# Kernel optimization log

Hardware: AMD Instinct MI355X
Metric: run time of the kernel (lower is better)

## Reference

```python
import jax, jax.numpy as jnp
import numpy as np

T_FINAL = 1.0
DT_STEP = 0.2
MSQ = 0.1
ALPHA = 0.0
CLIP = 1e8


def dt_to_matrix(dt):
    # dt: (H, W, 3) -> per-pixel 3x3 stencil weights (H, W, 1, 9)
    dt00 = dt
    dt01 = jnp.roll(dt00, 1, axis=1)
    dt10 = jnp.roll(dt00, 1, axis=0)
    dt11 = jnp.roll(dt01, 1, axis=0)
    dt_10 = jnp.roll(dt00, -1, axis=0)
    dt0_1 = jnp.roll(dt00, -1, axis=1)
    dt_1_1 = jnp.roll(dt_10, -1, axis=1)
    dt_11 = jnp.roll(dt_10, 1, axis=1)
    dt1_1 = jnp.roll(dt0_1, 1, axis=0)
    a00, c00, b00 = jnp.split(dt00, 3, axis=-1)
    a01, c01, b01 = jnp.split(dt01, 3, axis=-1)
    a10, c10, b10 = jnp.split(dt10, 3, axis=-1)
    a11, c11, b11 = jnp.split(dt11, 3, axis=-1)
    a0_1, c0_1, b0_1 = jnp.split(dt0_1, 3, axis=-1)
    a_10, c_10, b_10 = jnp.split(dt_10, 3, axis=-1)
    a_1_1, c_1_1, b_1_1 = jnp.split(dt_1_1, 3, axis=-1)
    a_11, c_11, b_11 = jnp.split(dt_11, 3, axis=-1)
    a1_1, c1_1, b1_1 = jnp.split(dt1_1, 3, axis=-1)
    A0 = (jnp.abs(b_11) - b_11 + jnp.abs(b00) - b00) / 4.0
    A1 = (c01 + c00 - jnp.abs(b01) - jnp.abs(b00)) / 2.0
    A2 = (jnp.abs(b11) + b11 + jnp.abs(b00) + b00) / 4.0
    A3 = (a_10 + a00 - jnp.abs(b_10) - jnp.abs(b00)) / 2.0
    A4 = (-(a_10 + 2 * a00 + a10) / 2.0
          - (jnp.abs(b_11) - b_11 + jnp.abs(b11) + b11) / 4.0
          - (jnp.abs(b_1_1) + b_1_1 + jnp.abs(b1_1) - b1_1) / 4.0
          + (jnp.abs(b_10) + jnp.abs(b10) + jnp.abs(b0_1) + jnp.abs(b01) + 2 * jnp.abs(b00)) / 2.0
          - (c0_1 + 2 * c00 + c01) / 2.0)
    A5 = (a10 + a00 - jnp.abs(b10) - jnp.abs(b00)) / 2.0
    A6 = (jnp.abs(b_1_1) + b_1_1 + jnp.abs(b00) + b00) / 4.0
    A7 = (c0_1 + c00 - jnp.abs(b0_1) - jnp.abs(b00)) / 2.0
    A8 = (jnp.abs(b1_1) - b1_1 + jnp.abs(b00) - b00) / 4.0
    return jnp.stack([A0, A1, A2, A3, A4, A5, A6, A7, A8], axis=-1)


def LB(dt, X):
    # per-pixel local 3x3 conv applied independently to each of the N channels
    A = dt_to_matrix(dt)  # (H, W, 1, 9)
    return jax.lax.conv_general_dilated_local(
        X[jnp.newaxis, ...], A, filter_shape=(3, 3), window_strides=(1, 1),
        padding='SAME', dimension_numbers=('CHWN', 'HWOI', 'CHWN'))[0]


def derivative(u):
    # forward finite differences via roll: (2, H, W, N)
    return jnp.stack([jnp.roll(u, -1, axis=0) - u, jnp.roll(u, -1, axis=1) - u])


def nrm(dt, v):
    # quadratic form: a*vx^2 + 2*b*vx*vy + c*vy^2, dt=(H,W,3), v=(2,H,W)
    return dt[:, :, 0] * v[0] ** 2 + 2 * dt[:, :, 2] * (v[1] * v[0]) + dt[:, :, 1] * v[1] ** 2


nrm2 = jax.vmap(nrm, in_axes=[None, -1], out_axes=-1)


def Pi_0(x):
    # projection onto zero-mean (simplex tangent) over channel axis
    return x - jnp.mean(x, axis=-1, keepdims=True)


def setup_inputs() -> dict:
    key = jax.random.key(0)
    k1, k2, k3, k4 = jax.random.split(key, 4)
    H, W, N = 512, 512, 48
    v = jax.random.normal(k1, (H, W, N), dtype=jnp.float32)
    Dt = jax.random.uniform(k2, (H, W, 3), dtype=jnp.float32)
    dg = jax.random.uniform(k3, (H, W, 1), dtype=jnp.float32) * 0.9 + 0.1
    hinv = jax.random.uniform(k4, (H, W, 3), dtype=jnp.float32)
    return {"v": v, "Dt": Dt, "dg": dg, "hinv": hinv}


def reference(v, Dt, dg, hinv):
    n_steps = int(T_FINAL / DT_STEP)  # 5 unrolled Euler steps

    def rhs(x):
        logp = jax.nn.log_softmax(x, axis=-1)
        val = LB(Dt, x) / dg + (1.0 - ALPHA) / 2.0 * nrm2(hinv, derivative(logp)) + MSQ * x
        return jnp.clip(Pi_0(val), -CLIP, CLIP)

    x = v
    for _ in range(n_steps):
        x = x + DT_STEP * rhs(x)
    return x
```

## Files before the change

### kernel.cpp

```cpp
#include <hip/hip_runtime.h>
#include <math.h>

#define HH 512
#define WW 512
#define NCH 48
#define HWPIX (HH * WW)

#define TW 16
#define TH 8
#define HW_HALO 18
#define HH_HALO 10
#define NHALO (HW_HALO * HH_HALO)
#define PSTRIDE 13
#define ASTRIDE 12

__global__ __launch_bounds__(256) void compute_A_kernel(
    const float* __restrict__ Dt, const float* __restrict__ dg,
    float* __restrict__ A) {
  int pix = blockIdx.x * blockDim.x + threadIdx.x;
  int h = pix >> 9;
  int w = pix & (WW - 1);
  int hm = (h == 0) ? HH - 1 : h - 1;
  int hp = (h == HH - 1) ? 0 : h + 1;
  int wm = (w == 0) ? WW - 1 : w - 1;
  int wp = (w == WW - 1) ? 0 : w + 1;

  float aC, cC, bC, cL, bL, cR, bR, aU, bU, aD, bD;
  float bUL, bUR, bDL, bDR;
  {
    int p;
    p = (h * WW + w) * 3;   aC = Dt[p]; cC = Dt[p + 1]; bC = Dt[p + 2];
    p = (h * WW + wm) * 3;  cL = Dt[p + 1]; bL = Dt[p + 2];
    p = (h * WW + wp) * 3;  cR = Dt[p + 1]; bR = Dt[p + 2];
    p = (hm * WW + w) * 3;  aU = Dt[p]; bU = Dt[p + 2];
    p = (hp * WW + w) * 3;  aD = Dt[p]; bD = Dt[p + 2];
    p = (hm * WW + wm) * 3; bUL = Dt[p + 2];
    p = (hm * WW + wp) * 3; bUR = Dt[p + 2];
    p = (hp * WW + wm) * 3; bDL = Dt[p + 2];
    p = (hp * WW + wp) * 3; bDR = Dt[p + 2];
  }

  float A0 = (fabsf(bDL) - bDL + fabsf(bC) - bC) * 0.25f;
  float A1 = (cL + cC - fabsf(bL) - fabsf(bC)) * 0.5f;
  float A2 = (fabsf(bUL) + bUL + fabsf(bC) + bC) * 0.25f;
  float A3 = (aD + aC - fabsf(bD) - fabsf(bC)) * 0.5f;
  float A4 = -(aD + 2.f * aC + aU) * 0.5f
             - (fabsf(bDL) - bDL + fabsf(bUL) + bUL) * 0.25f
             - (fabsf(bDR) + bDR + fabsf(bUR) - bUR) * 0.25f
             + (fabsf(bD) + fabsf(bU) + fabsf(bR) + fabsf(bL) + 2.f * fabsf(bC)) * 0.5f
             - (cR + 2.f * cC + cL) * 0.5f;
  float A5 = (aU + aC - fabsf(bU) - fabsf(bC)) * 0.5f;
  float A6 = (fabsf(bDR) + bDR + fabsf(bC) + bC) * 0.25f;
  float A7 = (cR + cC - fabsf(bR) - fabsf(bC)) * 0.5f;
  float A8 = (fabsf(bUR) - bUR + fabsf(bC) - bC) * 0.25f;

  bool ru = (h > 0), rd = (h < HH - 1), cl = (w > 0), cr = (w < WW - 1);
  if (!(ru && cl)) A0 = 0.f;
  if (!ru)         A1 = 0.f;
  if (!(ru && cr)) A2 = 0.f;
  if (!cl)         A3 = 0.f;
  if (!cr)         A5 = 0.f;
  if (!(rd && cl)) A6 = 0.f;
  if (!rd)         A7 = 0.f;
  if (!(rd && cr)) A8 = 0.f;

  float g = 1.0f / dg[pix];
  float4* Ao = (float4*)A + (size_t)pix * 3;
  Ao[0] = make_float4(A0 * g, A1 * g, A2 * g, A3 * g);
  Ao[1] = make_float4(A4 * g + 0.1f, A5 * g, A6 * g, A7 * g);
  Ao[2] = make_float4(A8 * g, 0.f, 0.f, 0.f);
}

__global__ __launch_bounds__(256, 4) void step_fused_kernel(
    const float* __restrict__ x, const float* __restrict__ A,
    const float* __restrict__ hinv, float* __restrict__ xn) {
  __shared__ float4 tile[NHALO * PSTRIDE];
  __shared__ float lse_s[NHALO];

  int b = blockIdx.x;
  int tile_id = (b & 7) * 256 + (b >> 3);
  int th0 = (tile_id >> 5) * TH;
  int tw0 = (tile_id & 31) * TW;

  int t = threadIdx.x;
  int sub = t & 3;
  int pair = t >> 2;
  int pr = pair >> 3;
  int pc0 = (pair & 7) * 2;
  int pix0 = (th0 + pr) * WW + (tw0 + pc0);
  int pix1 = pix0 + 1;

  float4 v[12];
  bool stager = (t < NHALO);
  if (stager) {
    int r = t / HW_HALO;
    int c = t - r * HW_HALO;
    int gh = (th0 + r - 1) & (HH - 1);
    int gw = (tw0 + c - 1) & (WW - 1);
    const float4* src = (const float4*)x + (size_t)(gh * WW + gw) * 12;
#pragma unroll
    for (int i = 0; i < 12; i++) v[i] = src[i];
  }

  const float4* ap0 = (const float4*)A + (size_t)pix0 * 3;
  const float4* ap1 = (const float4*)A + (size_t)pix1 * 3;
  float4 wA0 = ap0[0], wB0 = ap0[1], wC0 = ap0[2];
  float4 wA1 = ap1[0], wB1 = ap1[1], wC1 = ap1[2];
  const float2* hp = (const float2*)(hinv + (size_t)pix0 * 3);
  float2 h01 = hp[0], h23 = hp[1], h45 = hp[2];

  if (stager) {
    float4 mv = v[0];
#pragma unroll
    for (int i = 1; i < 12; i++) {
      mv.x = fmaxf(mv.x, v[i].x); mv.y = fmaxf(mv.y, v[i].y);
      mv.z = fmaxf(mv.z, v[i].z); mv.w = fmaxf(mv.w, v[i].w);
    }
    float m = fmaxf(fmaxf(mv.x, mv.y), fmaxf(mv.z, mv.w));
    float sx = 0.f, sy = 0.f, sz = 0.f, sw = 0.f;
#pragma unroll
    for (int i = 0; i < 12; i++) {
      sx += __expf(v[i].x - m); sy += __expf(v[i].y - m);
      sz += __expf(v[i].z - m); sw += __expf(v[i].w - m);
      tile[t * PSTRIDE + i] = v[i];
    }
    lse_s[t] = m + __logf((sx + sy) + (sz + sw));
  }
  __syncthreads();

  float wt0[9] = {wA0.x, wA0.y, wA0.z, wA0.w, wB0.x, wB0.y, wB0.z, wB0.w, wC0.x};
  float wt1[9] = {wA1.x, wA1.y, wA1.z, wA1.w, wB1.x, wB1.y, wB1.z, wB1.w, wC1.x};
  float ha0 = h01.x, hc0 = h01.y, hb0 = h23.x;
  float ha1 = h23.y, hc1 = h45.x, hb1 = h45.y;

  int lc0 = (pr + 1) * HW_HALO + (pc0 + 1);
  float l0C = lse_s[lc0];
  float l0R = lse_s[lc0 + 1];
  float l1R = lse_s[lc0 + 2];
  float l0D = lse_s[lc0 + HW_HALO];
  float l1D = lse_s[lc0 + HW_HALO + 1];
  float dld0 = l0C - l0D, dlr0 = l0C - l0R;
  float dld1 = l0R - l1D, dlr1 = l0R - l1R;

  int poff[3][4];
#pragma unroll
  for (int dr = 0; dr < 3; dr++)
#pragma unroll
    for (int dc = 0; dc < 4; dc++)
      poff[dr][dc] = ((pr + dr) * HW_HALO + pc0 + dc) * PSTRIDE;

  float4 vals0[3], vals1[3];
  float sum0 = 0.f, sum1 = 0.f;
#pragma unroll
  for (int j = 0; j < 3; j++) {
    int ch = j * 4 + sub;
    float4 q[3][4];
#pragma unroll
    for (int dr = 0; dr < 3; dr++)
#pragma unroll
      for (int dc = 0; dc < 4; dc++) q[dr][dc] = tile[poff[dr][dc] + ch];

    float4 val0, val1;
#define COMP(f)                                                                \
    {                                                                          \
      float s0_ = wt0[0] * q[0][0].f + wt0[1] * q[0][1].f + wt0[2] * q[0][2].f \
                + wt0[3] * q[1][0].f + wt0[4] * q[1][1].f + wt0[5] * q[1][2].f \
                + wt0[6] * q[2][0].f + wt0[7] * q[2][1].f + wt0[8] * q[2][2].f;\
      float v00 = q[2][1].f - q[1][1].f + dld0;                                \
      float v10 = q[1][2].f - q[1][1].f + dlr0;                                \
      float vv0 = s0_ + 0.5f * (ha0 * v00 * v00 + hc0 * v10 * v10) +           \
                  hb0 * (v00 * v10);                                           \
      val0.f = vv0; sum0 += vv0;                                               \
      float s1_ = wt1[0] * q[0][1].f + wt1[1] * q[0][2].f + wt1[2] * q[0][3].f \
                + wt1[3] * q[1][1].f + wt1[4] * q[1][2].f + wt1[5] * q[1][3].f \
                + wt1[6] * q[2][1].f + wt1[7] * q[2][2].f + wt1[8] * q[2][3].f;\
      float v01 = q[2][2].f - q[1][2].f + dld1;                                \
      float v11 = q[1][3].f - q[1][2].f + dlr1;                                \
      float vv1 = s1_ + 0.5f * (ha1 * v01 * v01 + hc1 * v11 * v11) +           \
                  hb1 * (v01 * v11);                                           \
      val1.f = vv1; sum1 += vv1;                                               \
    }
    COMP(x) COMP(y) COMP(z) COMP(w)
#undef COMP
    vals0[j] = val0;
    vals1[j] = val1;
  }

  sum0 += __shfl_xor(sum0, 1); sum0 += __shfl_xor(sum0, 2);
  sum1 += __shfl_xor(sum1, 1); sum1 += __shfl_xor(sum1, 2);
  float mean0 = sum0 * (1.0f / 48.0f);
  float mean1 = sum1 * (1.0f / 48.0f);

  int cen0 = lc0 * PSTRIDE;
  float4* op0 = (float4*)(xn + (size_t)pix0 * NCH);
  float4* op1 = op0 + 12;
#pragma unroll
  for (int j = 0; j < 3; j++) {
    int ch = j * 4 + sub;
    float4 c0 = tile[cen0 + ch];
    float4 c1 = tile[cen0 + PSTRIDE + ch];
    float4 r0, r1;
    r0.x = c0.x + 0.2f * fminf(fmaxf(vals0[j].x - mean0, -1e8f), 1e8f);
    r0.y = c0.y + 0.2f * fminf(fmaxf(vals0[j].y - mean0, -1e8f), 1e8f);
    r0.z = c0.z + 0.2f * fminf(fmaxf(vals0[j].z - mean0, -1e8f), 1e8f);
    r0.w = c0.w + 0.2f * fminf(fmaxf(vals0[j].w - mean0, -1e8f), 1e8f);
    r1.x = c1.x + 0.2f * fminf(fmaxf(vals1[j].x - mean1, -1e8f), 1e8f);
    r1.y = c1.y + 0.2f * fminf(fmaxf(vals1[j].y - mean1, -1e8f), 1e8f);
    r1.z = c1.z + 0.2f * fminf(fmaxf(vals1[j].z - mean1, -1e8f), 1e8f);
    r1.w = c1.w + 0.2f * fminf(fmaxf(vals1[j].w - mean1, -1e8f), 1e8f);
    op0[ch] = r0;
    op1[ch] = r1;
  }
}

extern "C" void kernel_launch(void* const* d_in, const int* in_sizes, int n_in,
                              void* d_out, int out_size, void* d_ws, size_t ws_size,
                              hipStream_t stream) {
  const float* v    = (const float*)d_in[0];
  const float* Dt   = (const float*)d_in[1];
  const float* dg   = (const float*)d_in[2];
  const float* hinv = (const float*)d_in[3];
  float* out = (float*)d_out;

  float* A    = (float*)d_ws;
  float* xbuf = A + (size_t)ASTRIDE * HWPIX;

  compute_A_kernel<<<dim3(HWPIX / 256), dim3(256), 0, stream>>>(Dt, dg, A);

  const float* cur = v;
  float* nxt = out;
  for (int s = 0; s < 5; s++) {
    step_fused_kernel<<<dim3(HWPIX / 128), dim3(256), 0, stream>>>(cur, A, hinv, nxt);
    if (s == 0) {
      cur = out;
      nxt = xbuf;
    } else {
      float* t = (float*)cur;
      cur = nxt;
      nxt = t;
    }
  }
}
```

Measured before the change: 209.8 us.

## Double-buffer two tiles per block with async global-to-LDS prefetch

```diff
diff --git a/kernel.cpp b/kernel.cpp
--- a/kernel.cpp
+++ b/kernel.cpp
@@ -11,8 +11,19 @@
 #define HW_HALO 18
 #define HH_HALO 10
 #define NHALO (HW_HALO * HH_HALO)
-#define PSTRIDE 13
 #define ASTRIDE 12
+
+#define BLK_STRIDE 65
+#define WAVE_STRIDE 780
+#define BUF_SLOTS (36 * BLK_STRIDE)
+
+#define NBLOCKS 1024
+
+__device__ __forceinline__ void gl2lds16(const float4* g, float4* l) {
+  __builtin_amdgcn_global_load_lds(
+      (const __attribute__((address_space(1))) void*)g,
+      (__attribute__((address_space(3))) void*)l, 16, 0, 0);
+}
 
 __global__ __launch_bounds__(256) void compute_A_kernel(
     const float* __restrict__ Dt, const float* __restrict__ dg,
@@ -71,67 +82,14 @@
   Ao[2] = make_float4(A8 * g, 0.f, 0.f, 0.f);
 }
 
-__global__ __launch_bounds__(256, 4) void step_fused_kernel(
-    const float* __restrict__ x, const float* __restrict__ A,
-    const float* __restrict__ hinv, float* __restrict__ xn) {
-  __shared__ float4 tile[NHALO * PSTRIDE];
-  __shared__ float lse_s[NHALO];
-
-  int b = blockIdx.x;
-  int tile_id = (b & 7) * 256 + (b >> 3);
-  int th0 = (tile_id >> 5) * TH;
-  int tw0 = (tile_id & 31) * TW;
-
-  int t = threadIdx.x;
-  int sub = t & 3;
-  int pair = t >> 2;
-  int pr = pair >> 3;
-  int pc0 = (pair & 7) * 2;
+__device__ __forceinline__ void phase2(
+    const float4* __restrict__ buf, const float* __restrict__ lse_s,
+    float* __restrict__ xn, int th0, int tw0,
+    int sub, int pr, int pc0,
+    const float* wt0, const float* wt1,
+    float ha0, float hc0, float hb0,
+    float ha1, float hc1, float hb1) {
   int pix0 = (th0 + pr) * WW + (tw0 + pc0);
-  int pix1 = pix0 + 1;
-
-  float4 v[12];
-  bool stager = (t < NHALO);
-  if (stager) {
-    int r = t / HW_HALO;
-    int c = t - r * HW_HALO;
-    int gh = (th0 + r - 1) & (HH - 1);
-    int gw = (tw0 + c - 1) & (WW - 1);
-    const float4* src = (const float4*)x + (size_t)(gh * WW + gw) * 12;
-#pragma unroll
-    for (int i = 0; i < 12; i++) v[i] = src[i];
-  }
-
-  const float4* ap0 = (const float4*)A + (size_t)pix0 * 3;
-  const float4* ap1 = (const float4*)A + (size_t)pix1 * 3;
-  float4 wA0 = ap0[0], wB0 = ap0[1], wC0 = ap0[2];
-  float4 wA1 = ap1[0], wB1 = ap1[1], wC1 = ap1[2];
-  const float2* hp = (const float2*)(hinv + (size_t)pix0 * 3);
-  float2 h01 = hp[0], h23 = hp[1], h45 = hp[2];
-
-  if (stager) {
-    float4 mv = v[0];
-#pragma unroll
-    for (int i = 1; i < 12; i++) {
-      mv.x = fmaxf(mv.x, v[i].x); mv.y = fmaxf(mv.y, v[i].y);
-      mv.z = fmaxf(mv.z, v[i].z); mv.w = fmaxf(mv.w, v[i].w);
-    }
-    float m = fmaxf(fmaxf(mv.x, mv.y), fmaxf(mv.z, mv.w));
-    float sx = 0.f, sy = 0.f, sz = 0.f, sw = 0.f;
-#pragma unroll
-    for (int i = 0; i < 12; i++) {
-      sx += __expf(v[i].x - m); sy += __expf(v[i].y - m);
-      sz += __expf(v[i].z - m); sw += __expf(v[i].w - m);
-      tile[t * PSTRIDE + i] = v[i];
-    }
-    lse_s[t] = m + __logf((sx + sy) + (sz + sw));
-  }
-  __syncthreads();
-
-  float wt0[9] = {wA0.x, wA0.y, wA0.z, wA0.w, wB0.x, wB0.y, wB0.z, wB0.w, wC0.x};
-  float wt1[9] = {wA1.x, wA1.y, wA1.z, wA1.w, wB1.x, wB1.y, wB1.z, wB1.w, wC1.x};
-  float ha0 = h01.x, hc0 = h01.y, hb0 = h23.x;
-  float ha1 = h23.y, hc1 = h45.x, hb1 = h45.y;
 
   int lc0 = (pr + 1) * HW_HALO + (pc0 + 1);
   float l0C = lse_s[lc0];
@@ -142,23 +100,26 @@
   float dld0 = l0C - l0D, dlr0 = l0C - l0R;
   float dld1 = l0R - l1D, dlr1 = l0R - l1R;
 
-  int poff[3][4];
+  int base4[3][4];
 #pragma unroll
   for (int dr = 0; dr < 3; dr++)
 #pragma unroll
-    for (int dc = 0; dc < 4; dc++)
-      poff[dr][dc] = ((pr + dr) * HW_HALO + pc0 + dc) * PSTRIDE;
+    for (int dc = 0; dc < 4; dc++) {
+      int p = (pr + dr) * HW_HALO + pc0 + dc;
+      base4[dr][dc] = (p >> 6) * WAVE_STRIDE + (p & 63);
+    }
 
   float4 vals0[3], vals1[3];
   float sum0 = 0.f, sum1 = 0.f;
 #pragma unroll
   for (int j = 0; j < 3; j++) {
     int ch = j * 4 + sub;
+    int choff = ch * BLK_STRIDE;
     float4 q[3][4];
 #pragma unroll
     for (int dr = 0; dr < 3; dr++)
 #pragma unroll
-      for (int dc = 0; dc < 4; dc++) q[dr][dc] = tile[poff[dr][dc] + ch];
+      for (int dc = 0; dc < 4; dc++) q[dr][dc] = buf[base4[dr][dc] + choff];
 
     float4 val0, val1;
 #define COMP(f)                                                                \
@@ -191,14 +152,17 @@
   float mean0 = sum0 * (1.0f / 48.0f);
   float mean1 = sum1 * (1.0f / 48.0f);
 
-  int cen0 = lc0 * PSTRIDE;
+  int cb0 = (lc0 >> 6) * WAVE_STRIDE + (lc0 & 63);
+  int lc1 = lc0 + 1;
+  int cb1 = (lc1 >> 6) * WAVE_STRIDE + (lc1 & 63);
   float4* op0 = (float4*)(xn + (size_t)pix0 * NCH);
   float4* op1 = op0 + 12;
 #pragma unroll
   for (int j = 0; j < 3; j++) {
     int ch = j * 4 + sub;
-    float4 c0 = tile[cen0 + ch];
-    float4 c1 = tile[cen0 + PSTRIDE + ch];
+    int choff = ch * BLK_STRIDE;
+    float4 c0 = buf[cb0 + choff];
+    float4 c1 = buf[cb1 + choff];
     float4 r0, r1;
     r0.x = c0.x + 0.2f * fminf(fmaxf(vals0[j].x - mean0, -1e8f), 1e8f);
     r0.y = c0.y + 0.2f * fminf(fmaxf(vals0[j].y - mean0, -1e8f), 1e8f);
@@ -213,6 +177,126 @@
   }
 }
 
+__global__ __launch_bounds__(256, 2) void step_fused_kernel(
+    const float* __restrict__ x, const float* __restrict__ A,
+    const float* __restrict__ hinv, float* __restrict__ xn) {
+  __shared__ float4 bufA[BUF_SLOTS];
+  __shared__ float4 bufB[BUF_SLOTS];
+  __shared__ float lseA[192];
+  __shared__ float lseB[192];
+
+  int b = blockIdx.x;
+  int tid0 = (b & 7) * 256 + (b >> 3);
+  int th0A = (tid0 >> 5) * TH;
+  int tw0A = (tid0 & 31) * TW;
+  int th0B = th0A + 32;
+  int tw0B = tw0A;
+
+  int t = threadIdx.x;
+  int sub = t & 3;
+  int pair = t >> 2;
+  int pr = pair >> 3;
+  int pc0 = (pair & 7) * 2;
+
+  bool stager = (t < NHALO);
+  int wv = t >> 6;
+  int r = t / HW_HALO;
+  int c = t - r * HW_HALO;
+  int lane = t & 63;
+
+  if (stager) {
+    int gh = (th0A + r - 1) & (HH - 1);
+    int gw = (tw0A + c - 1) & (WW - 1);
+    const float4* src = (const float4*)x + (size_t)(gh * WW + gw) * 12;
+    float4 v[12];
+#pragma unroll
+    for (int i = 0; i < 12; i++) v[i] = src[i];
+    float4 mv = v[0];
+#pragma unroll
+    for (int i = 1; i < 12; i++) {
+      mv.x = fmaxf(mv.x, v[i].x); mv.y = fmaxf(mv.y, v[i].y);
+      mv.z = fmaxf(mv.z, v[i].z); mv.w = fmaxf(mv.w, v[i].w);
+    }
+    float m = fmaxf(fmaxf(mv.x, mv.y), fmaxf(mv.z, mv.w));
+    float sx = 0.f, sy = 0.f, sz = 0.f, sw = 0.f;
+    float4* dst = bufA + wv * WAVE_STRIDE + lane;
+#pragma unroll
+    for (int i = 0; i < 12; i++) {
+      sx += __expf(v[i].x - m); sy += __expf(v[i].y - m);
+      sz += __expf(v[i].z - m); sw += __expf(v[i].w - m);
+      dst[i * BLK_STRIDE] = v[i];
+    }
+    lseA[t] = m + __logf((sx + sy) + (sz + sw));
+  }
+
+  int pixA0 = (th0A + pr) * WW + (tw0A + pc0);
+  const float4* apA0 = (const float4*)A + (size_t)pixA0 * 3;
+  const float4* apA1 = apA0 + 3;
+  float4 aA0 = apA0[0], aA1 = apA0[1], aA2 = apA0[2];
+  float4 bA0 = apA1[0], bA1 = apA1[1], bA2 = apA1[2];
+  const float2* hpA = (const float2*)(hinv + (size_t)pixA0 * 3);
+  float2 hA01 = hpA[0], hA23 = hpA[1], hA45 = hpA[2];
+
+  __syncthreads();
+
+  if (stager) {
+    int gh = (th0B + r - 1) & (HH - 1);
+    int gw = (tw0B + c - 1) & (WW - 1);
+    const float4* src = (const float4*)x + (size_t)(gh * WW + gw) * 12;
+    float4* dst = bufB + wv * WAVE_STRIDE;
+#pragma unroll
+    for (int i = 0; i < 12; i++)
+      gl2lds16(src + i, dst + i * BLK_STRIDE);
+  }
+
+  {
+    float wt0[9] = {aA0.x, aA0.y, aA0.z, aA0.w, aA1.x, aA1.y, aA1.z, aA1.w, aA2.x};
+    float wt1[9] = {bA0.x, bA0.y, bA0.z, bA0.w, bA1.x, bA1.y, bA1.z, bA1.w, bA2.x};
+    phase2(bufA, lseA, xn, th0A, tw0A, sub, pr, pc0, wt0, wt1,
+           hA01.x, hA01.y, hA23.x, hA23.y, hA45.x, hA45.y);
+  }
+
+  __syncthreads();
+
+  int pixB0 = (th0B + pr) * WW + (tw0B + pc0);
+  const float4* apB0 = (const float4*)A + (size_t)pixB0 * 3;
+  const float4* apB1 = apB0 + 3;
+  float4 aB0 = apB0[0], aB1 = apB0[1], aB2 = apB0[2];
+  float4 bB0 = apB1[0], bB1 = apB1[1], bB2 = apB1[2];
+  const float2* hpB = (const float2*)(hinv + (size_t)pixB0 * 3);
+  float2 hB01 = hpB[0], hB23 = hpB[1], hB45 = hpB[2];
+
+  if (stager) {
+    const float4* sp = bufB + wv * WAVE_STRIDE + lane;
+    float4 v[12];
+#pragma unroll
+    for (int i = 0; i < 12; i++) v[i] = sp[i * BLK_STRIDE];
+    float4 mv = v[0];
+#pragma unroll
+    for (int i = 1; i < 12; i++) {
+      mv.x = fmaxf(mv.x, v[i].x); mv.y = fmaxf(mv.y, v[i].y);
+      mv.z = fmaxf(mv.z, v[i].z); mv.w = fmaxf(mv.w, v[i].w);
+    }
+    float m = fmaxf(fmaxf(mv.x, mv.y), fmaxf(mv.z, mv.w));
+    float sx = 0.f, sy = 0.f, sz = 0.f, sw = 0.f;
+#pragma unroll
+    for (int i = 0; i < 12; i++) {
+      sx += __expf(v[i].x - m); sy += __expf(v[i].y - m);
+      sz += __expf(v[i].z - m); sw += __expf(v[i].w - m);
+    }
+    lseB[t] = m + __logf((sx + sy) + (sz + sw));
+  }
+
+  __syncthreads();
+
+  {
+    float wt0[9] = {aB0.x, aB0.y, aB0.z, aB0.w, aB1.x, aB1.y, aB1.z, aB1.w, aB2.x};
+    float wt1[9] = {bB0.x, bB0.y, bB0.z, bB0.w, bB1.x, bB1.y, bB1.z, bB1.w, bB2.x};
+    phase2(bufB, lseB, xn, th0B, tw0B, sub, pr, pc0, wt0, wt1,
+           hB01.x, hB01.y, hB23.x, hB23.y, hB45.x, hB45.y);
+  }
+}
+
 extern "C" void kernel_launch(void* const* d_in, const int* in_sizes, int n_in,
                               void* d_out, int out_size, void* d_ws, size_t ws_size,
                               hipStream_t stream) {
@@ -230,7 +314,7 @@
   const float* cur = v;
   float* nxt = out;
   for (int s = 0; s < 5; s++) {
-    step_fused_kernel<<<dim3(HWPIX / 128), dim3(256), 0, stream>>>(cur, A, hinv, nxt);
+    step_fused_kernel<<<dim3(NBLOCKS), dim3(256), 0, stream>>>(cur, A, hinv, nxt);
     if (s == 0) {
       cur = out;
       nxt = xbuf;
```

Result: slower. 233.0 us (+11.1%).
